# Optimization experiments

Measured on AMD Instinct MI355X. Metric: run time of the kernel, lower is better.

## Reference

```python
import jax, jax.numpy as jnp
import numpy as np

N = 100000   # nodes
E = 1600000  # edges (avg degree 16)
F = 64       # in_feats
H = 128      # hidden_size
O = 10       # out_feats
L = 3        # SAGEConv layers
EPS = 1e-5


def setup_inputs() -> dict:
    key = jax.random.key(0)
    ks = jax.random.split(key, 16)
    s = 0.05
    return {
        "nodes": jax.random.normal(ks[0], (N, F), jnp.float32),
        "src": jax.random.randint(ks[1], (E,), 0, N),
        "dst": jax.random.randint(ks[2], (E,), 0, N),
        # input MLP: Linear(F,H) -> ReLU -> Linear(H,H)
        "W_in1": jax.random.normal(ks[3], (F, H), jnp.float32) * s,
        "b_in1": jnp.zeros((H,), jnp.float32),
        "W_in2": jax.random.normal(ks[4], (H, H), jnp.float32) * s,
        "b_in2": jnp.zeros((H,), jnp.float32),
        # L stacked SAGEConv layers (mean aggregator)
        "W_self": jax.random.normal(ks[5], (L, H, H), jnp.float32) * s,
        "W_neigh": jax.random.normal(ks[6], (L, H, H), jnp.float32) * s,
        "b_sage": jnp.zeros((L, H), jnp.float32),
        "ln_g": jnp.ones((L, H), jnp.float32),
        "ln_b": jnp.zeros((L, H), jnp.float32),
        # output head Linear(H, O)
        "W_out": jax.random.normal(ks[7], (H, O), jnp.float32) * s,
        "b_out": jnp.zeros((O,), jnp.float32),
    }


def reference(nodes, src, dst, W_in1, b_in1, W_in2, b_in2,
              W_self, W_neigh, b_sage, ln_g, ln_b, W_out, b_out):
    # input MLP
    h = jax.nn.relu(nodes @ W_in1 + b_in1) @ W_in2 + b_in2  # [N, H]

    # in-degree for mean aggregation (0-degree nodes get 0 neighbor feature)
    deg = jax.ops.segment_sum(jnp.ones((E,), h.dtype), dst, num_segments=N)
    inv_deg = (1.0 / jnp.maximum(deg, 1.0))[:, None]  # [N, 1]

    for l in range(L):
        # mean over incoming neighbors: gather src feats, scatter-add to dst
        agg = jax.ops.segment_sum(h[src], dst, num_segments=N) * inv_deg  # [N, H]
        h = h @ W_self[l] + agg @ W_neigh[l] + b_sage[l]
        h = jax.nn.relu(h)
        # LayerNorm over feature dim
        mu = h.mean(-1, keepdims=True)
        var = h.var(-1, keepdims=True)
        h = ln_g[l] * (h - mu) * jax.lax.rsqrt(var + EPS) + ln_b[l]

    # dgl.mean_nodes over the single graph -> [1, H]
    g = h.mean(0, keepdims=True)
    return g @ W_out + b_out  # [1, O]
```

## Files before the change

### kernel.cpp

```cpp
#include <hip/hip_runtime.h>
#include <hip/hip_bf16.h>

#define NN 100000
#define NE 1600000
#define FF 64
#define HH 128
#define OO 10
#define NL 3
#define NB 391
#define NBLK 250
#define CHUNK 6400
#define BCAP 5376
#define LNEPS 1e-5f

typedef short s8v __attribute__((ext_vector_type(8)));
typedef float f32x4 __attribute__((ext_vector_type(4)));
typedef float f32x2 __attribute__((ext_vector_type(2)));

__device__ __forceinline__ unsigned short f2b(float f){
  unsigned u = __float_as_uint(f);
  unsigned r = (u + 0x7FFFu + ((u>>16)&1u)) >> 16;
  return (unsigned short)r;
}
__device__ __forceinline__ float b2f(unsigned short b){
  return __uint_as_float(((unsigned)b)<<16);
}

#if __has_builtin(__builtin_amdgcn_cvt_pk_f32_fp8) && __has_builtin(__builtin_amdgcn_cvt_pk_fp8_f32)
__device__ __forceinline__ unsigned char f8enc(float x){
  int p = __builtin_amdgcn_cvt_pk_fp8_f32(x, x, 0, false);
  return (unsigned char)(p & 0xFF);
}
__device__ __forceinline__ void f8dec4(unsigned u, float* o){
  f32x2 lo = __builtin_amdgcn_cvt_pk_f32_fp8(u, false);
  f32x2 hi = __builtin_amdgcn_cvt_pk_f32_fp8(u, true);
  o[0]=lo[0]; o[1]=lo[1]; o[2]=hi[0]; o[3]=hi[1];
}
#else
#include <hip/hip_fp8.h>
__device__ __forceinline__ unsigned char f8enc(float x){
  __hip_fp8_e4m3 q(x); return (unsigned char)q.__x;
}
__device__ __forceinline__ void f8dec4(unsigned u, float* o){
  for(int i=0;i<4;i++){
    __hip_fp8_e4m3 q; q.__x = (unsigned char)(u>>(8*i));
    o[i] = (float)q;
  }
}
#endif

__global__ __launch_bounds__(256) void k_bcount(const int* __restrict__ dst, int* __restrict__ bcnt,
                                                int* __restrict__ blockcnt){
  __shared__ int h[NB];
  for(int i=threadIdx.x;i<NB;i+=256) h[i]=0;
  __syncthreads();
  int base = blockIdx.x*CHUNK;
  for(int i=threadIdx.x;i<CHUNK;i+=256){
    int e = base+i;
    if(e<NE) atomicAdd(&h[((unsigned)dst[e])>>8],1);
  }
  __syncthreads();
  for(int i=threadIdx.x;i<NB;i+=256){
    int v=h[i];
    blockcnt[i*256 + blockIdx.x] = v;
    if(v) atomicAdd(&bcnt[i],v);
  }
}

__global__ void k_bscan(const int* __restrict__ bcnt, int* __restrict__ boff, int* __restrict__ rowoff){
  __shared__ int s[512];
  int t=threadIdx.x;
  int v = (t<NB)? bcnt[t]:0;
  s[t]=v; __syncthreads();
  for(int off=1;off<512;off<<=1){
    int x=(t>=off)?s[t-off]:0;
    __syncthreads();
    s[t]+=x;
    __syncthreads();
  }
  if(t<NB) boff[t]=s[t]-v;
  if(t==0) rowoff[NN]=NE;
}

__global__ void k_prefix(const int* __restrict__ blockcnt, const int* __restrict__ boff,
                         int* __restrict__ pref){
  __shared__ int s[256];
  int k=blockIdx.x, t=threadIdx.x;
  int v = (t<NBLK)? blockcnt[k*256+t] : 0;
  s[t]=v; __syncthreads();
  for(int off=1;off<256;off<<=1){
    int x=(t>=off)?s[t-off]:0;
    __syncthreads();
    s[t]+=x;
    __syncthreads();
  }
  if(t<NBLK) pref[k*256+t] = boff[k] + s[t]-v;
}

__global__ __launch_bounds__(256) void k_bscatter(const int* __restrict__ src, const int* __restrict__ dst,
                                                  const int* __restrict__ pref, unsigned* __restrict__ ebuf){
  __shared__ int cur[NB];
  __shared__ int pb[NB];
  for(int i=threadIdx.x;i<NB;i+=256){ cur[i]=0; pb[i]=pref[i*256+blockIdx.x]; }
  __syncthreads();
  int base=blockIdx.x*CHUNK;
  for(int i=threadIdx.x;i<CHUNK;i+=256){
    int e=base+i;
    if(e<NE){
      int d=dst[e];
      int k=((unsigned)d)>>8;
      int r=atomicAdd(&cur[k],1);
      ebuf[pb[k]+r] = (unsigned)src[e] | ((unsigned)(d&255)<<20);
    }
  }
}

__global__ __launch_bounds__(256) void k_bsort(const unsigned* __restrict__ ebuf, const int* __restrict__ bcnt,
                                               const int* __restrict__ boff, int* __restrict__ rowoff,
                                               float* __restrict__ invd, int* __restrict__ csr){
  __shared__ unsigned el[BCAP];
  __shared__ int dg[256], sc[256], cu[256];
  int b=blockIdx.x, t=threadIdx.x;
  int c = bcnt[b]; if(c>BCAP) c=BCAP;
  int base = boff[b];
  for(int i=t;i<c;i+=256) el[i]=ebuf[base+i];
  dg[t]=0;
  __syncthreads();
  for(int i=t;i<c;i+=256) atomicAdd(&dg[el[i]>>20],1);
  __syncthreads();
  int v = dg[t];
  sc[t]=v; __syncthreads();
  for(int off=1;off<256;off<<=1){
    int x=(t>=off)?sc[t-off]:0;
    __syncthreads();
    sc[t]+=x;
    __syncthreads();
  }
  int excl = sc[t]-v;
  int node = b*256+t;
  if(node<NN){
    rowoff[node]=base+excl;
    invd[node]=1.0f/fmaxf((float)v,1.0f);
  }
  cu[t]=excl;
  __syncthreads();
  for(int i=t;i<c;i+=256){
    unsigned e=el[i];
    int d=e>>20;
    int p=atomicAdd(&cu[d],1);
    csr[base+p] = (int)(e & 0xFFFFFu);
  }
}

__global__ void k_cvtin(const float* __restrict__ x, unsigned* __restrict__ xb, int n4){
  int i = blockIdx.x*256+threadIdx.x;
  if(i<n4){
    float4 v = *(const float4*)&x[i*4];
    uint2 p;
    p.x = (unsigned)f2b(v.x) | ((unsigned)f2b(v.y)<<16);
    p.y = (unsigned)f2b(v.z) | ((unsigned)f2b(v.w)<<16);
    *(uint2*)&xb[i*2] = p;
  }
}

__global__ void k_repack(const float* __restrict__ W1, const float* __restrict__ W2,
                         const float* __restrict__ Ws, const float* __restrict__ Wn,
                         unsigned short* __restrict__ wf){
  int t = blockIdx.x*256+threadIdx.x;
  if(t >= 122880) return;
  const float* src; int rem;
  if(t < 8192){ src = W1; rem = t; }
  else {
    int u = t - 8192;
    int m = u >> 14; rem = u & 16383;
    if(m==0) src = W2;
    else if(m<=3) src = Ws + (size_t)(m-1)*HH*HH;
    else src = Wn + (size_t)(m-4)*HH*HH;
  }
  int j = rem&7, l=(rem>>3)&63, nt=(rem>>9)&7, kcb=rem>>12;
  int k = kcb*32 + 8*(l>>4) + j;
  int n = nt*16 + (l&15);
  wf[t] = f2b(src[(size_t)k*HH + n]);
}

__global__ __launch_bounds__(256) void k_agg(const uint2* __restrict__ hf8, const int* __restrict__ csr,
                                             const int* __restrict__ rowoff, const float* __restrict__ invd,
                                             uint4* __restrict__ aggb){
  int wave=threadIdx.x>>6, lane=threadIdx.x&63;
  int n = blockIdx.x*4+wave;
  if(n>=NN) return;
  int beg=rowoff[n], end=rowoff[n+1];
  int c = lane&15, q=lane>>4;
  float a0=0.f,a1=0.f,a2=0.f,a3=0.f,a4=0.f,a5=0.f,a6=0.f,a7=0.f;
  int j=beg;
  for(; j+4<=end; j+=4){
    int s0=csr[j+q];
    uint2 u=hf8[(size_t)s0*16+c];
    float d0[4], d1[4];
    f8dec4(u.x,d0); f8dec4(u.y,d1);
    a0+=d0[0]; a1+=d0[1]; a2+=d0[2]; a3+=d0[3];
    a4+=d1[0]; a5+=d1[1]; a6+=d1[2]; a7+=d1[3];
  }
  if(j<end){
    if(j+q<end){
      int s0=csr[j+q];
      uint2 u=hf8[(size_t)s0*16+c];
      float d0[4], d1[4];
      f8dec4(u.x,d0); f8dec4(u.y,d1);
      a0+=d0[0]; a1+=d0[1]; a2+=d0[2]; a3+=d0[3];
      a4+=d1[0]; a5+=d1[1]; a6+=d1[2]; a7+=d1[3];
    }
  }
  a0+=__shfl_xor(a0,16); a1+=__shfl_xor(a1,16); a2+=__shfl_xor(a2,16); a3+=__shfl_xor(a3,16);
  a4+=__shfl_xor(a4,16); a5+=__shfl_xor(a5,16); a6+=__shfl_xor(a6,16); a7+=__shfl_xor(a7,16);
  a0+=__shfl_xor(a0,32); a1+=__shfl_xor(a1,32); a2+=__shfl_xor(a2,32); a3+=__shfl_xor(a3,32);
  a4+=__shfl_xor(a4,32); a5+=__shfl_xor(a5,32); a6+=__shfl_xor(a6,32); a7+=__shfl_xor(a7,32);
  if(q==0){
    float s=invd[n];
    uint4 p;
    p.x = (unsigned)f2b(a0*s) | ((unsigned)f2b(a1*s)<<16);
    p.y = (unsigned)f2b(a2*s) | ((unsigned)f2b(a3*s)<<16);
    p.z = (unsigned)f2b(a4*s) | ((unsigned)f2b(a5*s)<<16);
    p.w = (unsigned)f2b(a6*s) | ((unsigned)f2b(a7*s)<<16);
    aggb[(size_t)n*16 + c] = p;
  }
}

template<int K, int DUAL, int RELU, int LN, int F8, int MEAN>
__global__ __launch_bounds__(256) void k_mfma(
    const unsigned short* __restrict__ A, const unsigned short* __restrict__ A2,
    const unsigned short* __restrict__ Wf, const unsigned short* __restrict__ Wf2,
    const float* __restrict__ bias, const float* __restrict__ lng, const float* __restrict__ lnb,
    unsigned short* __restrict__ out, unsigned char* __restrict__ hf8, float* __restrict__ gsum)
{
  constexpr int KC = K/32;
  __shared__ unsigned short Wl[KC*8*64*8];
  __shared__ unsigned short Wl2[DUAL ? KC*8*64*8 : 8];
  __shared__ float sm[MEAN ? 4*128 : 4];
  int tid = threadIdx.x;
  {
    const int tot = KC*8*64*8/8;
    for(int i=tid;i<tot;i+=256){
      ((uint4*)Wl)[i] = ((const uint4*)Wf)[i];
      if(DUAL) ((uint4*)Wl2)[i] = ((const uint4*)Wf2)[i];
    }
  }
  __syncthreads();
  int l = tid&63, wv = tid>>6;
  int grp = l>>4, lc = l&15;
  int node0 = blockIdx.x*64 + wv*16;
  int arow = node0 + lc; if(arow > NN-1) arow = NN-1;
  f32x4 acc[8] = {};
  const s8v* Wv  = (const s8v*)Wl;
  const s8v* Wv2 = (const s8v*)Wl2;
  #pragma unroll
  for(int kcb=0;kcb<KC;kcb++){
    s8v a = *(const s8v*)&A[(size_t)arow*K + kcb*32 + 8*grp];
    s8v a2;
    if(DUAL) a2 = *(const s8v*)&A2[(size_t)arow*K + kcb*32 + 8*grp];
    #pragma unroll
    for(int nt=0;nt<8;nt++){
      acc[nt] = __builtin_amdgcn_mfma_f32_16x16x32_bf16(a, Wv[(kcb*8+nt)*64 + l], acc[nt], 0,0,0);
      if(DUAL)
        acc[nt] = __builtin_amdgcn_mfma_f32_16x16x32_bf16(a2, Wv2[(kcb*8+nt)*64 + l], acc[nt], 0,0,0);
    }
  }
  float bc[8], gc[8], oc[8];
  #pragma unroll
  for(int nt=0;nt<8;nt++){
    bc[nt] = bias[nt*16+lc];
    if(LN){ gc[nt]=lng[nt*16+lc]; oc[nt]=lnb[nt*16+lc]; }
  }
  float msum[8];
  #pragma unroll
  for(int nt=0;nt<8;nt++) msum[nt]=0.f;
  #pragma unroll
  for(int r=0;r<4;r++){
    float x[8]; float s=0.f, ss=0.f;
    #pragma unroll
    for(int nt=0;nt<8;nt++){
      float v = acc[nt][r] + bc[nt];
      if(RELU) v = fmaxf(v, 0.f);
      x[nt]=v; s+=v; ss+=v*v;
    }
    if(LN){
      #pragma unroll
      for(int m=1;m<=8;m<<=1){ s+=__shfl_xor(s,m); ss+=__shfl_xor(ss,m); }
      float mu = s*(1.0f/HH);
      float var = ss*(1.0f/HH) - mu*mu;
      float rs = rsqrtf(var + LNEPS);
      #pragma unroll
      for(int nt=0;nt<8;nt++) x[nt] = gc[nt]*(x[nt]-mu)*rs + oc[nt];
    }
    int node = node0 + grp*4 + r;
    if(node<NN){
      if(MEAN){
        #pragma unroll
        for(int nt=0;nt<8;nt++) msum[nt]+=x[nt];
      } else {
        #pragma unroll
        for(int nt=0;nt<8;nt++) out[(size_t)node*HH + nt*16 + lc] = f2b(x[nt]);
        if(F8){
          #pragma unroll
          for(int nt=0;nt<8;nt++) hf8[(size_t)node*HH + nt*16 + lc] = f8enc(x[nt]);
        }
      }
    }
  }
  if(MEAN){
    #pragma unroll
    for(int nt=0;nt<8;nt++){
      msum[nt]+=__shfl_xor(msum[nt],16);
      msum[nt]+=__shfl_xor(msum[nt],32);
    }
    if(grp==0){
      #pragma unroll
      for(int nt=0;nt<8;nt++) sm[wv*128 + nt*16 + lc] = msum[nt];
    }
    __syncthreads();
    if(tid<128){
      float v = sm[tid] + sm[128+tid] + sm[256+tid] + sm[384+tid];
      atomicAdd(&gsum[tid], v);
    }
  }
}

__global__ void k_out(const float* __restrict__ g, const float* __restrict__ Wout,
                      const float* __restrict__ bout, float* __restrict__ out){
  int o=threadIdx.x;
  if(o<OO){
    float acc=bout[o];
    for(int k=0;k<HH;k++) acc = fmaf(g[k]*(1.0f/NN), Wout[k*OO+o], acc);
    out[o]=acc;
  }
}

extern "C" void kernel_launch(void* const* d_in, const int* in_sizes, int n_in,
                              void* d_out, int out_size, void* d_ws, size_t ws_size,
                              hipStream_t stream){
  const float* nodes = (const float*)d_in[0];
  const int*   src   = (const int*)d_in[1];
  const int*   dst   = (const int*)d_in[2];
  const float* W_in1 = (const float*)d_in[3];
  const float* b_in1 = (const float*)d_in[4];
  const float* W_in2 = (const float*)d_in[5];
  const float* b_in2 = (const float*)d_in[6];
  const float* W_self  = (const float*)d_in[7];
  const float* W_neigh = (const float*)d_in[8];
  const float* b_sage  = (const float*)d_in[9];
  const float* ln_g    = (const float*)d_in[10];
  const float* ln_b    = (const float*)d_in[11];
  const float* W_out   = (const float*)d_in[12];
  const float* b_out   = (const float*)d_in[13];

  char* w=(char*)d_ws;
  unsigned short* hb   = (unsigned short*)w; w += (size_t)NN*HH*2;
  unsigned short* aggb = (unsigned short*)w; w += (size_t)NN*HH*2;
  unsigned short* xb   = (unsigned short*)w; w += (size_t)NN*FF*2;
  unsigned char*  hf8  = (unsigned char*)w;  w += (size_t)NN*HH;
  unsigned short* wf   = (unsigned short*)w; w += (size_t)122880*2;
  unsigned* ebuf = (unsigned*)w; w += (size_t)NE*4;
  int* csr    = (int*)w;   w += (size_t)NE*4;
  int* rowoff = (int*)w;   w += (size_t)(NN+8)*4;
  float* invd = (float*)w; w += (size_t)NN*4;
  int* bcnt   = (int*)w;   w += (size_t)(NB+1)*4;
  int* boff   = (int*)w;   w += (size_t)(NB+1)*4;
  int* blockcnt=(int*)w;   w += (size_t)NB*256*4;
  int* pref   = (int*)w;   w += (size_t)NB*256*4;
  float* gsum = (float*)w; w += 128*4;

  hipMemsetAsync(bcnt, 0, (size_t)(NB+1)*4, stream);
  hipMemsetAsync(gsum, 0, 128*4, stream);

  k_bcount<<<NBLK,256,0,stream>>>(dst,bcnt,blockcnt);
  k_bscan<<<1,512,0,stream>>>(bcnt,boff,rowoff);
  k_prefix<<<NB,256,0,stream>>>(blockcnt,boff,pref);
  k_bscatter<<<NBLK,256,0,stream>>>(src,dst,pref,ebuf);
  k_bsort<<<NB,256,0,stream>>>(ebuf,bcnt,boff,rowoff,invd,csr);

  k_cvtin<<<((NN*FF/4)+255)/256,256,0,stream>>>(nodes,(unsigned*)xb, NN*FF/4);
  k_repack<<<(122880+255)/256,256,0,stream>>>(W_in1,W_in2,W_self,W_neigh,wf);

  const int GB = (NN+63)/64;
  k_mfma<FF,0,1,0,0,0><<<GB,256,0,stream>>>(xb,nullptr, wf, nullptr, b_in1,nullptr,nullptr, aggb, nullptr, nullptr);
  k_mfma<HH,0,0,0,1,0><<<GB,256,0,stream>>>(aggb,nullptr, wf+8192, nullptr, b_in2,nullptr,nullptr, hb, hf8, nullptr);

  for(int l=0;l<NL;l++){
    k_agg<<<(NN+3)/4,256,0,stream>>>((const uint2*)hf8,csr,rowoff,invd,(uint4*)aggb);
    if(l<NL-1)
      k_mfma<HH,1,1,1,1,0><<<GB,256,0,stream>>>(hb, aggb,
          wf+24576+(size_t)l*16384, wf+73728+(size_t)l*16384,
          b_sage+(size_t)l*HH, ln_g+(size_t)l*HH, ln_b+(size_t)l*HH, hb, hf8, nullptr);
    else
      k_mfma<HH,1,1,1,0,1><<<GB,256,0,stream>>>(hb, aggb,
          wf+24576+(size_t)l*16384, wf+73728+(size_t)l*16384,
          b_sage+(size_t)l*HH, ln_g+(size_t)l*HH, ln_b+(size_t)l*HH, hb, nullptr, gsum);
  }
  k_out<<<1,64,0,stream>>>(gsum,W_out,b_out,(float*)d_out);
}
```

Baseline: 404.2 us.

## Drop LDS weight staging in MFMA GEMM and process two row tiles per wave

```diff
diff --git a/kernel.cpp b/kernel.cpp
--- a/kernel.cpp
+++ b/kernel.cpp
@@ -234,35 +234,35 @@
     unsigned short* __restrict__ out, unsigned char* __restrict__ hf8, float* __restrict__ gsum)
 {
   constexpr int KC = K/32;
-  __shared__ unsigned short Wl[KC*8*64*8];
-  __shared__ unsigned short Wl2[DUAL ? KC*8*64*8 : 8];
   __shared__ float sm[MEAN ? 4*128 : 4];
   int tid = threadIdx.x;
-  {
-    const int tot = KC*8*64*8/8;
-    for(int i=tid;i<tot;i+=256){
-      ((uint4*)Wl)[i] = ((const uint4*)Wf)[i];
-      if(DUAL) ((uint4*)Wl2)[i] = ((const uint4*)Wf2)[i];
-    }
-  }
-  __syncthreads();
   int l = tid&63, wv = tid>>6;
   int grp = l>>4, lc = l&15;
-  int node0 = blockIdx.x*64 + wv*16;
-  int arow = node0 + lc; if(arow > NN-1) arow = NN-1;
-  f32x4 acc[8] = {};
-  const s8v* Wv  = (const s8v*)Wl;
-  const s8v* Wv2 = (const s8v*)Wl2;
+  int node0 = blockIdx.x*128;
+  const s8v* __restrict__ Wv  = (const s8v*)Wf;
+  const s8v* __restrict__ Wv2 = (const s8v*)Wf2;
+  f32x4 acc[2][8] = {};
+  int r0 = node0 + wv*16 + lc;      if(r0>NN-1) r0=NN-1;
+  int r1 = node0 + 64 + wv*16 + lc; if(r1>NN-1) r1=NN-1;
   #pragma unroll
   for(int kcb=0;kcb<KC;kcb++){
-    s8v a = *(const s8v*)&A[(size_t)arow*K + kcb*32 + 8*grp];
-    s8v a2;
-    if(DUAL) a2 = *(const s8v*)&A2[(size_t)arow*K + kcb*32 + 8*grp];
+    s8v a0 = *(const s8v*)&A[(size_t)r0*K + kcb*32 + 8*grp];
+    s8v a1 = *(const s8v*)&A[(size_t)r1*K + kcb*32 + 8*grp];
+    s8v c0, c1;
+    if(DUAL){
+      c0 = *(const s8v*)&A2[(size_t)r0*K + kcb*32 + 8*grp];
+      c1 = *(const s8v*)&A2[(size_t)r1*K + kcb*32 + 8*grp];
+    }
     #pragma unroll
     for(int nt=0;nt<8;nt++){
-      acc[nt] = __builtin_amdgcn_mfma_f32_16x16x32_bf16(a, Wv[(kcb*8+nt)*64 + l], acc[nt], 0,0,0);
-      if(DUAL)
-        acc[nt] = __builtin_amdgcn_mfma_f32_16x16x32_bf16(a2, Wv2[(kcb*8+nt)*64 + l], acc[nt], 0,0,0);
+      s8v b = Wv[(kcb*8+nt)*64 + l];
+      acc[0][nt] = __builtin_amdgcn_mfma_f32_16x16x32_bf16(a0, b, acc[0][nt], 0,0,0);
+      acc[1][nt] = __builtin_amdgcn_mfma_f32_16x16x32_bf16(a1, b, acc[1][nt], 0,0,0);
+      if(DUAL){
+        s8v b2 = Wv2[(kcb*8+nt)*64 + l];
+        acc[0][nt] = __builtin_amdgcn_mfma_f32_16x16x32_bf16(c0, b2, acc[0][nt], 0,0,0);
+        acc[1][nt] = __builtin_amdgcn_mfma_f32_16x16x32_bf16(c1, b2, acc[1][nt], 0,0,0);
+      }
     }
   }
   float bc[8], gc[8], oc[8];
@@ -275,34 +275,37 @@
   #pragma unroll
   for(int nt=0;nt<8;nt++) msum[nt]=0.f;
   #pragma unroll
-  for(int r=0;r<4;r++){
-    float x[8]; float s=0.f, ss=0.f;
+  for(int s2=0;s2<2;s2++){
     #pragma unroll
-    for(int nt=0;nt<8;nt++){
-      float v = acc[nt][r] + bc[nt];
-      if(RELU) v = fmaxf(v, 0.f);
-      x[nt]=v; s+=v; ss+=v*v;
-    }
-    if(LN){
+    for(int r=0;r<4;r++){
+      float x[8]; float s=0.f, ss=0.f;
       #pragma unroll
-      for(int m=1;m<=8;m<<=1){ s+=__shfl_xor(s,m); ss+=__shfl_xor(ss,m); }
-      float mu = s*(1.0f/HH);
-      float var = ss*(1.0f/HH) - mu*mu;
-      float rs = rsqrtf(var + LNEPS);
-      #pragma unroll
-      for(int nt=0;nt<8;nt++) x[nt] = gc[nt]*(x[nt]-mu)*rs + oc[nt];
-    }
-    int node = node0 + grp*4 + r;
-    if(node<NN){
-      if(MEAN){
+      for(int nt=0;nt<8;nt++){
+        float v = acc[s2][nt][r] + bc[nt];
+        if(RELU) v = fmaxf(v, 0.f);
+        x[nt]=v; s+=v; ss+=v*v;
+      }
+      if(LN){
         #pragma unroll
-        for(int nt=0;nt<8;nt++) msum[nt]+=x[nt];
-      } else {
+        for(int m=1;m<=8;m<<=1){ s+=__shfl_xor(s,m); ss+=__shfl_xor(ss,m); }
+        float mu = s*(1.0f/HH);
+        float var = ss*(1.0f/HH) - mu*mu;
+        float rs = rsqrtf(var + LNEPS);
         #pragma unroll
-        for(int nt=0;nt<8;nt++) out[(size_t)node*HH + nt*16 + lc] = f2b(x[nt]);
-        if(F8){
+        for(int nt=0;nt<8;nt++) x[nt] = gc[nt]*(x[nt]-mu)*rs + oc[nt];
+      }
+      int node = node0 + s2*64 + wv*16 + grp*4 + r;
+      if(node<NN){
+        if(MEAN){
           #pragma unroll
-          for(int nt=0;nt<8;nt++) hf8[(size_t)node*HH + nt*16 + lc] = f8enc(x[nt]);
+          for(int nt=0;nt<8;nt++) msum[nt]+=x[nt];
+        } else {
+          #pragma unroll
+          for(int nt=0;nt<8;nt++) out[(size_t)node*HH + nt*16 + lc] = f2b(x[nt]);
+          if(F8){
+            #pragma unroll
+            for(int nt=0;nt<8;nt++) hf8[(size_t)node*HH + nt*16 + lc] = f8enc(x[nt]);
+          }
         }
       }
     }
@@ -381,18 +384,18 @@
   k_cvtin<<<((NN*FF/4)+255)/256,256,0,stream>>>(nodes,(unsigned*)xb, NN*FF/4);
   k_repack<<<(122880+255)/256,256,0,stream>>>(W_in1,W_in2,W_self,W_neigh,wf);
 
-  const int GB = (NN+63)/64;
-  k_mfma<FF,0,1,0,0,0><<<GB,256,0,stream>>>(xb,nullptr, wf, nullptr, b_in1,nullptr,nullptr, aggb, nullptr, nullptr);
-  k_mfma<HH,0,0,0,1,0><<<GB,256,0,stream>>>(aggb,nullptr, wf+8192, nullptr, b_in2,nullptr,nullptr, hb, hf8, nullptr);
+  const int GB2 = (NN+127)/128;
+  k_mfma<FF,0,1,0,0,0><<<GB2,256,0,stream>>>(xb,nullptr, wf, nullptr, b_in1,nullptr,nullptr, aggb, nullptr, nullptr);
+  k_mfma<HH,0,0,0,1,0><<<GB2,256,0,stream>>>(aggb,nullptr, wf+8192, nullptr, b_in2,nullptr,nullptr, hb, hf8, nullptr);
 
   for(int l=0;l<NL;l++){
     k_agg<<<(NN+3)/4,256,0,stream>>>((const uint2*)hf8,csr,rowoff,invd,(uint4*)aggb);
     if(l<NL-1)
-      k_mfma<HH,1,1,1,1,0><<<GB,256,0,stream>>>(hb, aggb,
+      k_mfma<HH,1,1,1,1,0><<<GB2,256,0,stream>>>(hb, aggb,
           wf+24576+(size_t)l*16384, wf+73728+(size_t)l*16384,
           b_sage+(size_t)l*HH, ln_g+(size_t)l*HH, ln_b+(size_t)l*HH, hb, hf8, nullptr);
     else
-      k_mfma<HH,1,1,1,0,1><<<GB,256,0,stream>>>(hb, aggb,
+      k_mfma<HH,1,1,1,0,1><<<GB2,256,0,stream>>>(hb, aggb,
           wf+24576+(size_t)l*16384, wf+73728+(size_t)l*16384,
           b_sage+(size_t)l*HH, ln_g+(size_t)l*HH, ln_b+(size_t)l*HH, hb, nullptr, gsum);
   }
```

Measured after the change: 400.5 us. Within noise of the previous version (-0.9%).
